# Optimization experiments

Measured on AMD Instinct MI355X. Metric: run time of the kernel, lower is better.

The kernel has to match this reference:

```python
import jax, jax.numpy as jnp
import numpy as np

N = 8192      # number of graph nodes (acts as 'batch')
HID = 1024    # hidden_size
HEADS = 16    # num_heads
DK = HID // HEADS
FFN = 4096    # ffn_size
OUT = 512     # out_size
SCALE = DK ** (-0.5)
EPS = 1e-5


def _layernorm(x, g, b):
    m = jnp.mean(x, axis=-1, keepdims=True)
    v = jnp.mean(jnp.square(x - m), axis=-1, keepdims=True)
    return (x - m) * jax.lax.rsqrt(v + EPS) * g + b


def setup_inputs() -> dict:
    key = jax.random.key(0)
    ks = jax.random.split(key, 24)
    s = 0.02
    f32 = jnp.float32
    inp = {
        'A':  jax.random.normal(ks[0], (N, N), f32) * (1.0 / np.sqrt(N)),
        'q':  jax.random.normal(ks[1], (N, HID), f32),
        'k':  jax.random.normal(ks[2], (N, HID), f32),
        'v1': jax.random.normal(ks[3], (N, HID), f32),
        'v2': jax.random.normal(ks[4], (N, HID), f32),
        # attention projections (note: v1 and v2 share linear_v in the original)
        'Wq': jax.random.normal(ks[5], (HID, HID), f32) * s, 'bq': jnp.zeros((HID,), f32),
        'Wk': jax.random.normal(ks[6], (HID, HID), f32) * s, 'bk': jnp.zeros((HID,), f32),
        'Wv': jax.random.normal(ks[7], (HID, HID), f32) * s, 'bv': jnp.zeros((HID,), f32),
        'Wo': jax.random.normal(ks[8], (HID, HID), f32) * s, 'bo': jnp.zeros((HID,), f32),
        # ffn_norm (self_attention_norm is declared but unused in the original forward)
        'ln_g': jnp.ones((HID,), f32), 'ln_b': jnp.zeros((HID,), f32),
        # FFN
        'W1': jax.random.normal(ks[9], (FFN, HID), f32) * s, 'b1': jnp.zeros((FFN,), f32),
        'W2': jax.random.normal(ks[10], (HID, FFN), f32) * s, 'b2': jnp.zeros((HID,), f32),
        # final fc
        'Wfc': jax.random.normal(ks[11], (OUT, HID), f32) * s, 'bfc': jnp.zeros((OUT,), f32),
    }
    return inp


def reference(A, q, k, v1, v2, Wq, bq, Wk, bk, Wv, bv, Wo, bo,
              ln_g, ln_b, W1, b1, W2, b2, Wfc, bfc):
    # --- new_MultiHeadAttention ---
    qh  = (q  @ Wq.T + bq).reshape(N, HEADS, DK)   # seq dim of 1 squeezed
    kh  = (k  @ Wk.T + bk).reshape(N, HEADS, DK)
    v1h = (v1 @ Wv.T + bv).reshape(N, HEADS, DK)
    v2h = (v2 @ Wv.T + bv).reshape(N, HEADS, DK)
    # per-node, per-head scalar score q.k (seq_len == 1)
    scores = jnp.einsum('nhd,nhd->nh', qh * SCALE, kh)          # (N, H)
    x = A @ scores                                              # (N, H) graph mixing
    # softmax over the size-1 seq dim -> all-ones weights (faithful to original)
    w = jax.nn.softmax(x[:, :, None, None], axis=3)             # (N, H, 1, 1)
    att = w[:, :, 0, :] * (v1h + v2h)                           # (N, H, DK)
    h_att = att.reshape(N, HID) @ Wo.T + bo                     # (N, HID)
    # --- residual average + FFN block ---
    h = h_att + (q + k + v1 + v2) * 0.25
    y = _layernorm(h, ln_g, ln_b)
    y = jax.nn.gelu(y @ W1.T + b1, approximate=False) @ W2.T + b2
    xres = h + y
    return xres @ Wfc.T + bfc                                   # (N, OUT)
```

## Files before the change

kernel.cpp:

```cpp
#include <hip/hip_runtime.h>
#include <math.h>

typedef __attribute__((ext_vector_type(8))) short     short8;
typedef __attribute__((ext_vector_type(4))) float     floatx4;
typedef __attribute__((ext_vector_type(8))) unsigned short ushort8v;
typedef __attribute__((ext_vector_type(4))) unsigned short ushort4v;
typedef __attribute__((ext_vector_type(4))) float     float4v;

__device__ __forceinline__ float b2f(unsigned short b) {
    unsigned u = ((unsigned)b) << 16;
    float f;
    __builtin_memcpy(&f, &u, 4);
    return f;
}
__device__ __forceinline__ unsigned short f2b(float f) {
    unsigned u;
    __builtin_memcpy(&u, &f, 4);
    u += 0x7fff + ((u >> 16) & 1);
    return (unsigned short)(u >> 16);
}

__device__ __forceinline__ int is_f32(const unsigned* lng) {
    return lng[0] == 0x3F800000u;
}

__device__ __forceinline__ void gl_lds16(const unsigned short* g, unsigned short* l) {
    __builtin_amdgcn_global_load_lds(
        (const __attribute__((address_space(1))) void*)g,
        (__attribute__((address_space(3))) void*)l,
        16, 0, 0);
}

__global__ __launch_bounds__(256)
void cvt_w(const void* s0, const void* s1, const void* s2, const void* s3,
           unsigned short* d0, unsigned short* d1, unsigned short* d2,
           unsigned short* d3,
           const unsigned* __restrict__ lng)
{
    const int f32in = is_f32(lng);
    size_t i = ((size_t)blockIdx.x * 256 + threadIdx.x) * 4;
    const size_t c0 = 1048576, c1 = 5242880, c2 = 9437184, c3 = 9961472;
    if (i >= c3) return;
    const void* s; unsigned short* d; size_t off;
    if      (i < c0) { s = s0; d = d0; off = i; }
    else if (i < c1) { s = s1; d = d1; off = i - c0; }
    else if (i < c2) { s = s2; d = d2; off = i - c1; }
    else             { s = s3; d = d3; off = i - c2; }
    ushort4v o;
    if (f32in) {
        float4v v = *(const float4v*)((const float*)s + off);
        o[0] = f2b(v[0]); o[1] = f2b(v[1]); o[2] = f2b(v[2]); o[3] = f2b(v[3]);
    } else {
        o = *(const ushort4v*)((const unsigned short*)s + off);
    }
    *(ushort4v*)(d + off) = o;
}

__global__ __launch_bounds__(256)
void cvt_wt(const void* __restrict__ src, unsigned short* __restrict__ dst,
            const unsigned* __restrict__ lng)
{
    __shared__ unsigned short t[32][33];
    const int f32in = is_f32(lng);
    const int r0 = blockIdx.y * 32, c0 = blockIdx.x * 32;
    const int tx = threadIdx.x & 31, ty = threadIdx.x >> 5;
#pragma unroll
    for (int r = ty; r < 32; r += 8) {
        unsigned short v;
        if (f32in) v = f2b(((const float*)src)[(size_t)(r0 + r) * 1024 + c0 + tx]);
        else       v = ((const unsigned short*)src)[(size_t)(r0 + r) * 1024 + c0 + tx];
        t[r][tx] = v;
    }
    __syncthreads();
#pragma unroll
    for (int r = ty; r < 32; r += 8)
        dst[(size_t)(c0 + r) * 1024 + r0 + tx] = t[tx][r];
}

__global__ __launch_bounds__(256)
void cvt_s(const void* s0, const void* s1, const void* s2, const void* s3,
           const void* s4, const void* s5, const void* s6,
           unsigned short* d)
{
    const int f32in = is_f32((const unsigned*)s5);
    size_t i = ((size_t)blockIdx.x * 256 + threadIdx.x) * 4;
    const size_t c0 = 1024, c1 = 2048, c2 = 6144, c3 = 7168, c4 = 7680, c5 = 8704, c6 = 9728;
    if (i >= c6) return;
    const void* s; size_t off;
    if      (i < c0) { s = s0; off = i; }
    else if (i < c1) { s = s1; off = i - c0; }
    else if (i < c2) { s = s2; off = i - c1; }
    else if (i < c3) { s = s3; off = i - c2; }
    else if (i < c4) { s = s4; off = i - c3; }
    else if (i < c5) { s = s5; off = i - c4; }
    else             { s = s6; off = i - c5; }
    ushort4v o;
    if (f32in) {
        float4v v = *(const float4v*)((const float*)s + off);
        o[0] = f2b(v[0]); o[1] = f2b(v[1]); o[2] = f2b(v[2]); o[3] = f2b(v[3]);
    } else {
        o = *(const ushort4v*)((const unsigned short*)s + off);
    }
    *(ushort4v*)(d + i) = o;
}

__global__ __launch_bounds__(256)
void bias_comb(const unsigned short* __restrict__ Wo,
               const unsigned short* __restrict__ bv,
               const unsigned short* __restrict__ bo,
               unsigned short* __restrict__ bc)
{
    const int n = blockIdx.x;
    const int tid = threadIdx.x;
    ushort4v w = *(const ushort4v*)(Wo + (size_t)n * 1024 + tid * 4);
    ushort4v b = *(const ushort4v*)(bv + tid * 4);
    float s = b2f(w[0]) * b2f(b[0]) + b2f(w[1]) * b2f(b[1])
            + b2f(w[2]) * b2f(b[2]) + b2f(w[3]) * b2f(b[3]);
#pragma unroll
    for (int off = 32; off > 0; off >>= 1) s += __shfl_down(s, off);
    __shared__ float red[4];
    const int wv = tid >> 6, lane = tid & 63;
    if (lane == 0) red[wv] = s;
    __syncthreads();
    if (tid == 0)
        bc[n] = f2b(2.0f * (red[0] + red[1] + red[2] + red[3]) + b2f(bo[n]));
}

template<int EPI>
__global__ __launch_bounds__(256)
void gemm_bt(const unsigned short* __restrict__ A,
             const unsigned short* __restrict__ B,
             unsigned short* __restrict__ C,
             const unsigned short* __restrict__ bias,
             float bscale,
             const unsigned short* __restrict__ add,
             const unsigned* __restrict__ ofl,
             int M, int N, int K)
{
    __shared__ unsigned short sA[128 * 32];
    __shared__ unsigned short sB[128 * 32];

    const int tid  = threadIdx.x;
    const int lane = tid & 63;
    const int w    = tid >> 6;
    const int bm   = blockIdx.x * 128;
    const int bn   = blockIdx.y * 128;
    const int wr   = (w >> 1) * 64;
    const int wc   = (w & 1) * 64;

    const floatx4 vzero = {0.f, 0.f, 0.f, 0.f};
    floatx4 acc[4][4];
#pragma unroll
    for (int i = 0; i < 4; ++i)
#pragma unroll
        for (int j = 0; j < 4; ++j) acc[i][j] = vzero;

    const int e0 = (w * 2 + 0) * 512 + lane * 8;
    const int e1 = (w * 2 + 1) * 512 + lane * 8;
    const int r0 = e0 >> 5, c0 = e0 & 31;
    const int r1 = e1 >> 5, c1 = e1 & 31;

    const unsigned short* gA0 = A + (size_t)(bm + r0) * K + c0;
    const unsigned short* gA1 = A + (size_t)(bm + r1) * K + c1;
    const unsigned short* gB0 = B + (size_t)(bn + r0) * K + c0;
    const unsigned short* gB1 = B + (size_t)(bn + r1) * K + c1;
    unsigned short* lA0 = sA + e0;
    unsigned short* lA1 = sA + e1;
    unsigned short* lB0 = sB + e0;
    unsigned short* lB1 = sB + e1;

    const int ln16 = lane & 15;
    const int qd   = lane >> 4;
    const unsigned short* pa = sA + (wr + ln16) * 32 + qd * 8;
    const unsigned short* pb = sB + (wc + ln16) * 32 + qd * 8;

    for (int k0 = 0; k0 < K; k0 += 32) {
        gl_lds16(gA0, lA0); gl_lds16(gA1, lA1);
        gl_lds16(gB0, lB0); gl_lds16(gB1, lB1);
        gA0 += 32; gA1 += 32; gB0 += 32; gB1 += 32;
        __syncthreads();

        short8 af[4], bfr[4];
#pragma unroll
        for (int t = 0; t < 4; ++t) {
            af[t]  = *(const short8*)(pa + t * 512);
            bfr[t] = *(const short8*)(pb + t * 512);
        }
#pragma unroll
        for (int mt = 0; mt < 4; ++mt)
#pragma unroll
            for (int nt = 0; nt < 4; ++nt)
                acc[mt][nt] = __builtin_amdgcn_mfma_f32_16x16x32_bf16(
                    af[mt], bfr[nt], acc[mt][nt], 0, 0, 0);
        __syncthreads();
    }

    const int of = ofl ? (ofl[0] == 0x3F800000u) : 0;

#pragma unroll
    for (int mt = 0; mt < 4; ++mt) {
#pragma unroll
        for (int nt = 0; nt < 4; ++nt) {
            const int col = bn + wc + nt * 16 + ln16;
            const float bb = b2f(bias[col]) * bscale;
#pragma unroll
            for (int r = 0; r < 4; ++r) {
                const int row = bm + wr + mt * 16 + qd * 4 + r;
                float v = acc[mt][nt][r] + bb;
                if (EPI == 1) v += b2f(add[(size_t)row * N + col]);
                if (EPI == 2) v = 0.5f * v * (1.0f + erff(v * 0.70710678118654752f));
                const size_t idx = (size_t)row * N + col;
                if (of) ((float*)C)[idx] = v;
                else    C[idx] = f2b(v);
            }
        }
    }
}

__global__ __launch_bounds__(256)
void ew_pre(const void* __restrict__ q,
            const void* __restrict__ k,
            const void* __restrict__ v1,
            const void* __restrict__ v2,
            unsigned short* __restrict__ vsum,
            unsigned short* __restrict__ r,
            const unsigned* __restrict__ lng)
{
    const int f32in = is_f32(lng);
    const size_t i = ((size_t)blockIdx.x * 256 + threadIdx.x) * 8;
    float fa[8], fb[8], fc[8], fd[8];
    if (f32in) {
        const float* qf = (const float*)q;  const float* kf = (const float*)k;
        const float* af = (const float*)v1; const float* bf = (const float*)v2;
#pragma unroll
        for (int j = 0; j < 8; j += 4) {
            float4v x0 = *(const float4v*)(qf + i + j);
            float4v x1 = *(const float4v*)(kf + i + j);
            float4v x2 = *(const float4v*)(af + i + j);
            float4v x3 = *(const float4v*)(bf + i + j);
#pragma unroll
            for (int t = 0; t < 4; ++t) { fa[j+t]=x0[t]; fb[j+t]=x1[t]; fc[j+t]=x2[t]; fd[j+t]=x3[t]; }
        }
    } else {
        ushort8v a = *(const ushort8v*)((const unsigned short*)q  + i);
        ushort8v b = *(const ushort8v*)((const unsigned short*)k  + i);
        ushort8v c = *(const ushort8v*)((const unsigned short*)v1 + i);
        ushort8v d = *(const ushort8v*)((const unsigned short*)v2 + i);
#pragma unroll
        for (int j = 0; j < 8; ++j) { fa[j]=b2f(a[j]); fb[j]=b2f(b[j]); fc[j]=b2f(c[j]); fd[j]=b2f(d[j]); }
    }
    ushort8v vs, rr;
#pragma unroll
    for (int j = 0; j < 8; ++j) {
        const float fv = fc[j] + fd[j];
        vs[j] = f2b(fv);
        rr[j] = f2b(0.25f * (fa[j] + fb[j] + fv));
    }
    *(ushort8v*)(vsum + i) = vs;
    *(ushort8v*)(r    + i) = rr;
}

__global__ __launch_bounds__(256)
void ln_kernel(const unsigned short* __restrict__ h,
               const unsigned short* __restrict__ g,
               const unsigned short* __restrict__ b,
               unsigned short* __restrict__ y)
{
    const int row = blockIdx.x;
    const int tid = threadIdx.x;
    const unsigned short* hr = h + (size_t)row * 1024;

    ushort4v hv = *(const ushort4v*)(hr + tid * 4);
    float x0 = b2f(hv[0]), x1 = b2f(hv[1]), x2 = b2f(hv[2]), x3 = b2f(hv[3]);
    float s  = x0 + x1 + x2 + x3;
    float s2 = x0 * x0 + x1 * x1 + x2 * x2 + x3 * x3;

#pragma unroll
    for (int off = 32; off > 0; off >>= 1) {
        s  += __shfl_down(s, off);
        s2 += __shfl_down(s2, off);
    }
    __shared__ float red[8];
    const int wv = tid >> 6, lane = tid & 63;
    if (lane == 0) { red[wv] = s; red[4 + wv] = s2; }
    __syncthreads();
    if (tid == 0) {
        red[0] = red[0] + red[1] + red[2] + red[3];
        red[4] = red[4] + red[5] + red[6] + red[7];
    }
    __syncthreads();
    const float mean = red[0] * (1.0f / 1024.0f);
    const float var  = red[4] * (1.0f / 1024.0f) - mean * mean;
    const float rstd = rsqrtf(var + 1e-5f);

    ushort4v gv = *(const ushort4v*)(g + tid * 4);
    ushort4v bv = *(const ushort4v*)(b + tid * 4);
    ushort4v ov;
    ov[0] = f2b((x0 - mean) * rstd * b2f(gv[0]) + b2f(bv[0]));
    ov[1] = f2b((x1 - mean) * rstd * b2f(gv[1]) + b2f(bv[1]));
    ov[2] = f2b((x2 - mean) * rstd * b2f(gv[2]) + b2f(bv[2]));
    ov[3] = f2b((x3 - mean) * rstd * b2f(gv[3]) + b2f(bv[3]));
    *(ushort4v*)(y + (size_t)row * 1024 + tid * 4) = ov;
}

extern "C" void kernel_launch(void* const* d_in, const int* in_sizes, int n_in,
                              void* d_out, int out_size, void* d_ws, size_t ws_size,
                              hipStream_t stream)
{
    const void* q   = d_in[1];
    const void* k   = d_in[2];
    const void* v1  = d_in[3];
    const void* v2  = d_in[4];
    const void* Wv  = d_in[9];
    const void* bv  = d_in[10];
    const void* Wo  = d_in[11];
    const void* bo  = d_in[12];
    const void* lng = d_in[13];
    const void* lnb = d_in[14];
    const void* W1  = d_in[15];
    const void* b1  = d_in[16];
    const void* W2  = d_in[17];
    const void* b2  = d_in[18];
    const void* Wfc = d_in[19];
    const void* bfc = d_in[20];

    const int N = 8192, HID = 1024, FFN = 4096, OUT = 512;
    const unsigned* lng_u = (const unsigned*)lng;

    char* p = (char*)d_ws;
    auto carve = [&](size_t bytes) {
        char* r = p;
        p += (bytes + 255) & ~(size_t)255;
        return r;
    };
    unsigned short* Wo_c   = (unsigned short*)carve((size_t)HID * HID * 2);
    unsigned short* W1_c   = (unsigned short*)carve((size_t)FFN * HID * 2);
    unsigned short* W2_c   = (unsigned short*)carve((size_t)HID * FFN * 2);
    unsigned short* Wfc_c  = (unsigned short*)carve((size_t)OUT * HID * 2);
    unsigned short* WvT_c  = (unsigned short*)carve((size_t)HID * HID * 2);
    unsigned short* Wc     = (unsigned short*)carve((size_t)HID * HID * 2);
    unsigned short* bc     = (unsigned short*)carve((size_t)HID * 2);
    unsigned short* smalls = (unsigned short*)carve(9728 * 2);
    unsigned short* bv_c   = smalls;
    unsigned short* bo_c   = smalls + 1024;
    unsigned short* b1_c   = smalls + 2048;
    unsigned short* b2_c   = smalls + 6144;
    unsigned short* bfc_c  = smalls + 7168;
    unsigned short* lng_c  = smalls + 7680;
    unsigned short* lnb_c  = smalls + 8704;
    unsigned short* vsum_y = (unsigned short*)carve((size_t)N * HID * 2);
    unsigned short* hbuf   = (unsigned short*)carve((size_t)N * HID * 2);
    unsigned short* xres   = (unsigned short*)carve((size_t)N * HID * 2);
    unsigned short* gbuf   = (unsigned short*)carve((size_t)N * FFN * 2);
    unsigned short* rbuf   = gbuf;

    dim3 blk(256);

    cvt_w<<<dim3(9728), blk, 0, stream>>>(Wo, W1, W2, Wfc,
                                          Wo_c, W1_c, W2_c, Wfc_c, lng_u);
    cvt_wt<<<dim3(32, 32), blk, 0, stream>>>(Wv, WvT_c, lng_u);
    cvt_s<<<dim3(10), blk, 0, stream>>>(bv, bo, b1, b2, bfc, lng, lnb, smalls);

    bias_comb<<<dim3(HID), blk, 0, stream>>>(Wo_c, bv_c, bo_c, bc);
    gemm_bt<0><<<dim3(HID / 128, HID / 128), blk, 0, stream>>>(
        Wo_c, WvT_c, Wc, bv_c, 0.0f, nullptr, nullptr, HID, HID, HID);

    ew_pre<<<dim3((N * HID) / (256 * 8)), blk, 0, stream>>>(q, k, v1, v2, vsum_y, rbuf, lng_u);

    gemm_bt<1><<<dim3(N / 128, HID / 128), blk, 0, stream>>>(
        vsum_y, Wc, hbuf, bc, 1.0f, rbuf, nullptr, N, HID, HID);

    ln_kernel<<<dim3(N), blk, 0, stream>>>(hbuf, lng_c, lnb_c, vsum_y);

    gemm_bt<2><<<dim3(N / 128, FFN / 128), blk, 0, stream>>>(
        vsum_y, W1_c, gbuf, b1_c, 1.0f, nullptr, nullptr, N, FFN, HID);

    gemm_bt<1><<<dim3(N / 128, HID / 128), blk, 0, stream>>>(
        gbuf, W2_c, xres, b2_c, 1.0f, hbuf, nullptr, N, HID, FFN);

    gemm_bt<0><<<dim3(N / 128, OUT / 128), blk, 0, stream>>>(
        xres, Wfc_c, (unsigned short*)d_out, bfc_c, 1.0f, nullptr, lng_u, N, OUT, HID);
}
```

Measured before the change: 802.9 us.

## Add 256x256 pipelined GELU GEMM for FFN up-projection and swizzle block order

Replaces the 128x128 GEMM used for the W1 projection with a new 512-thread kernel that computes 256x256 tiles. It uses direct global-to-LDS loads, double buffering with a 64-wide K step, XOR-swizzled LDS reads, and s_setprio around the MFMA bursts. The existing gemm_bt also remaps block indices in groups of eight, likely to spread neighbouring tiles across XCDs and improve L2 locality. The goal is more data reuse per tile and overlap of loads with compute, at the cost of heavy LDS use (128KB) and lower occupancy.

```diff
diff --git a/kernel.cpp b/kernel.cpp
--- a/kernel.cpp
+++ b/kernel.cpp
@@ -143,8 +143,18 @@
     const int tid  = threadIdx.x;
     const int lane = tid & 63;
     const int w    = tid >> 6;
-    const int bm   = blockIdx.x * 128;
-    const int bn   = blockIdx.y * 128;
+
+    int bx, by;
+    {
+        const int gx  = gridDim.x;
+        const int nb  = gx * gridDim.y;
+        const int n0  = blockIdx.y * gx + blockIdx.x;
+        const int cpx = nb >> 3;
+        const int sw  = (n0 & 7) * cpx + (n0 >> 3);
+        bx = sw % gx; by = sw / gx;
+    }
+    const int bm   = bx * 128;
+    const int bn   = by * 128;
     const int wr   = (w >> 1) * 64;
     const int wc   = (w & 1) * 64;
 
@@ -215,6 +225,138 @@
             }
         }
     }
+}
+
+__global__ __launch_bounds__(512, 2)
+void gemm256_gelu(const unsigned short* __restrict__ A,
+                  const unsigned short* __restrict__ B,
+                  unsigned short* __restrict__ C,
+                  const unsigned short* __restrict__ bias,
+                  int M, int N, int K)
+{
+    __shared__ __align__(16) unsigned short lds[65536];
+
+    const int tid  = threadIdx.x;
+    const int lane = tid & 63;
+    const int w    = tid >> 6;
+    const int wm   = w >> 2;
+    const int wn   = w & 3;
+    const int r16  = lane & 15;
+    const int qd   = lane >> 4;
+
+    const int nwg  = gridDim.x;
+    const int cpx  = nwg >> 3;
+    const int b0   = blockIdx.x;
+    const int bid  = (b0 & 7) * cpx + (b0 >> 3);
+    const int ntn  = N >> 8;
+    const int bm   = (bid / ntn) << 8;
+    const int bn   = (bid % ntn) << 8;
+
+    const int NT = K >> 6;
+
+    const int sxe    = ((lane >> 2) & 1) << 4;
+    const int a_base = (wm * 64 + r16) * 64 + ((qd * 8) ^ sxe);
+    const int b_base = (wn * 32 + r16) * 64 + ((qd * 8) ^ sxe);
+
+    const int lxe = (lane * 8) ^ (((lane >> 5) & 1) << 4);
+    const int ldl = lane * 8;
+
+    floatx4 acc[2][4][2][2];
+#pragma unroll
+    for (int a = 0; a < 2; ++a)
+#pragma unroll
+        for (int b = 0; b < 4; ++b)
+#pragma unroll
+            for (int c = 0; c < 2; ++c)
+#pragma unroll
+                for (int d = 0; d < 2; ++d)
+                    acc[a][b][c][d] = (floatx4){0.f, 0.f, 0.f, 0.f};
+
+    auto STG = [&](int mat, int tau, int h) {
+        if (tau >= NT) return;
+        const unsigned short* G = mat ? B : A;
+        const int row0 = mat ? bn : bm;
+        const int k0 = tau << 6;
+        unsigned short* base = lds + (mat ? 32768 : 0) + (tau & 1) * 16384;
+#pragma unroll
+        for (int tt = 0; tt < 2; ++tt) {
+            const int Es = h * 8192 + tt * 4096 + w * 512 + lxe;
+            const int rr = Es >> 6, cc = Es & 63;
+            const unsigned short* src = G + (size_t)(row0 + rr) * K + (k0 + cc);
+            unsigned short* dst = base + h * 8192 + tt * 4096 + w * 512 + ldl;
+            gl_lds16(src, dst);
+        }
+    };
+
+    STG(0, 0, 0); STG(1, 0, 0); STG(0, 0, 1); STG(1, 0, 1);
+    STG(0, 1, 0); STG(1, 1, 0);
+    asm volatile("s_waitcnt vmcnt(4)" ::: "memory");
+    __builtin_amdgcn_s_barrier();
+
+    for (int t = 0; t < NT; ++t) {
+        const unsigned short* Abuf = lds + (t & 1) * 16384;
+        const unsigned short* Bbuf = lds + 32768 + (t & 1) * 16384;
+#pragma unroll
+        for (int q = 0; q < 4; ++q) {
+            const int mg = q >> 1, ng = q & 1;
+            short8 afr[4][2], bfr[2][2];
+            const unsigned short* Ab = Abuf + mg * 8192 + a_base;
+            const unsigned short* Bb = Bbuf + ng * 8192 + b_base;
+#pragma unroll
+            for (int m = 0; m < 4; ++m)
+#pragma unroll
+                for (int kk = 0; kk < 2; ++kk)
+                    afr[m][kk] = *(const short8*)(Ab + m * 1024 + kk * 32);
+#pragma unroll
+            for (int n = 0; n < 2; ++n)
+#pragma unroll
+                for (int kk = 0; kk < 2; ++kk)
+                    bfr[n][kk] = *(const short8*)(Bb + n * 1024 + kk * 32);
+
+            if      (q == 0) STG(0, t + 1, 1);
+            else if (q == 1) STG(1, t + 1, 1);
+            else if (q == 2) STG(0, t + 2, 0);
+            else             STG(1, t + 2, 0);
+
+            __builtin_amdgcn_s_barrier();
+            asm volatile("s_waitcnt lgkmcnt(0)" ::: "memory");
+            __builtin_amdgcn_sched_barrier(0);
+            __builtin_amdgcn_s_setprio(1);
+#pragma unroll
+            for (int m = 0; m < 4; ++m)
+#pragma unroll
+                for (int n = 0; n < 2; ++n)
+#pragma unroll
+                    for (int kk = 0; kk < 2; ++kk)
+                        acc[mg][m][ng][n] = __builtin_amdgcn_mfma_f32_16x16x32_bf16(
+                            afr[m][kk], bfr[n][kk], acc[mg][m][ng][n], 0, 0, 0);
+            __builtin_amdgcn_s_setprio(0);
+            if (q == 3) {
+                if (t + 2 < NT) { asm volatile("s_waitcnt vmcnt(4)" ::: "memory"); }
+                else            { asm volatile("s_waitcnt vmcnt(0)" ::: "memory"); }
+            }
+            __builtin_amdgcn_s_barrier();
+        }
+    }
+
+#pragma unroll
+    for (int mg = 0; mg < 2; ++mg)
+#pragma unroll
+        for (int m = 0; m < 4; ++m)
+#pragma unroll
+            for (int ng = 0; ng < 2; ++ng)
+#pragma unroll
+                for (int n = 0; n < 2; ++n) {
+                    const int col = bn + ng * 128 + wn * 32 + n * 16 + r16;
+                    const float bb = b2f(bias[col]);
+#pragma unroll
+                    for (int r = 0; r < 4; ++r) {
+                        const int row = bm + mg * 128 + wm * 64 + m * 16 + qd * 4 + r;
+                        float v = acc[mg][m][ng][n][r] + bb;
+                        v = 0.5f * v * (1.0f + erff(v * 0.70710678118654752f));
+                        C[(size_t)row * N + col] = f2b(v);
+                    }
+                }
 }
 
 __global__ __launch_bounds__(256)
@@ -372,8 +514,8 @@
 
     ln_kernel<<<dim3(N), blk, 0, stream>>>(hbuf, lng_c, lnb_c, vsum_y);
 
-    gemm_bt<2><<<dim3(N / 128, FFN / 128), blk, 0, stream>>>(
-        vsum_y, W1_c, gbuf, b1_c, 1.0f, nullptr, nullptr, N, FFN, HID);
+    gemm256_gelu<<<dim3((N / 256) * (FFN / 256)), dim3(512), 0, stream>>>(
+        vsum_y, W1_c, gbuf, b1_c, N, FFN, HID);
 
     gemm_bt<1><<<dim3(N / 128, HID / 128), blk, 0, stream>>>(
         gbuf, W2_c, xres, b2_c, 1.0f, hbuf, nullptr, N, HID, FFN);
```

New measurement: 860.1 us. +7.1%, slower.
